# Kernel tuning notes

Measured on AMD Instinct MI355X. Metric: run time of the kernel, lower is better.

## Reference

```python
import jax, jax.numpy as jnp
import numpy as np

NUM_ANCHORS = 400_000
NUM_GTS = 64
NUM_CLASSES = 1
TOPK = 10
ALPHA = 1.0
BETA = 6.0
IMG = 640.0


def setup_inputs() -> dict:
    key = jax.random.key(0)
    k1, k2, k3, k4, k5, k6 = jax.random.split(key, 6)
    # anchor points uniformly over the image plane
    anc_points = jax.random.uniform(k1, (NUM_ANCHORS, 2), jnp.float32, 0.0, IMG)
    # predicted boxes: centered near the anchor point, valid xyxy
    pd_wh = jax.random.uniform(k2, (NUM_ANCHORS, 2), jnp.float32, 8.0, 96.0)
    pd_bboxes = jnp.concatenate([anc_points - pd_wh * 0.5, anc_points + pd_wh * 0.5], axis=-1)
    # predicted class scores in [0, 1] (post-sigmoid)
    pd_scores = jax.random.uniform(k3, (NUM_ANCHORS, NUM_CLASSES), jnp.float32)
    # GT boxes: random centers / sizes, valid xyxy
    gt_c = jax.random.uniform(k4, (NUM_GTS, 2), jnp.float32, 64.0, IMG - 64.0)
    gt_wh = jax.random.uniform(k5, (NUM_GTS, 2), jnp.float32, 16.0, 128.0)
    gt_bboxes = jnp.concatenate([gt_c - gt_wh * 0.5, gt_c + gt_wh * 0.5], axis=-1)
    gt_labels = jax.random.randint(k6, (NUM_GTS,), 0, NUM_CLASSES, dtype=jnp.int32)
    return {
        "pd_scores": pd_scores,
        "pd_bboxes": pd_bboxes,
        "anc_points": anc_points,
        "gt_labels": gt_labels,
        "gt_bboxes": gt_bboxes,
    }


def _box_iou(b1, b2):
    # b1: [A,4] xyxy, b2: [G,4] xyxy -> [A,G] pairwise IoU (torchvision box_iou math)
    lt = jnp.maximum(b1[:, None, :2], b2[None, :, :2])  # [A,G,2]
    rb = jnp.minimum(b1[:, None, 2:], b2[None, :, 2:])  # [A,G,2]
    wh = jnp.clip(rb - lt, 0.0)
    inter = wh[..., 0] * wh[..., 1]                      # [A,G]
    area1 = (b1[:, 2] - b1[:, 0]) * (b1[:, 3] - b1[:, 1])
    area2 = (b2[:, 2] - b2[:, 0]) * (b2[:, 3] - b2[:, 1])
    return inter / (area1[:, None] + area2[None, :] - inter)


def reference(pd_scores, pd_bboxes, anc_points, gt_labels, gt_bboxes):
    A = anc_points.shape[0]
    G = gt_bboxes.shape[0]
    # is anchor point inside each GT box -> [A,G] bool
    x, y = anc_points[:, 0:1], anc_points[:, 1:2]
    is_in_gts = ((x >= gt_bboxes[None, :, 0]) & (x <= gt_bboxes[None, :, 2]) &
                 (y >= gt_bboxes[None, :, 1]) & (y <= gt_bboxes[None, :, 3]))
    # Original gathers candidate anchors (inside >=1 GT) then computes metrics.
    # Equivalent dense form: non-candidates have is_in_gts row all-False so their
    # alignment metric is 0 for every GT and they are filtered by metric>0 below.
    iou = _box_iou(pd_bboxes, gt_bboxes)                         # [A,G]
    cls_scores = pd_scores[:, gt_labels]                          # [A,G]
    cls_scores = cls_scores * is_in_gts.astype(cls_scores.dtype)
    metric = (cls_scores ** ALPHA) * (iou ** BETA)                # [A,G]
    # per-GT top-k anchors by alignment metric
    _, topk_idx = jax.lax.top_k(metric.T, TOPK)                   # [G,k]
    topk_mask = jnp.zeros((A, G), dtype=bool)
    topk_mask = topk_mask.at[topk_idx.T, jnp.arange(G)[None, :]].set(True)
    topk_mask = topk_mask & (metric > 0)
    is_assigned = topk_mask.any(axis=1)                           # [A]
    best_gt = jnp.argmax(metric, axis=1)                          # [A]
    fg_mask = is_assigned
    assigned_gt_idx = jnp.where(fg_mask, best_gt, 0).astype(jnp.int32)
    return fg_mask, assigned_gt_idx
```

## Files before the change

kernel.cpp:

```cpp
#include <hip/hip_runtime.h>

#define NUM_A    400000
#define NUM_G    64
#define TOPK     10
#define CHUNKS   64
#define CHUNK_SZ (NUM_A / CHUNKS)
#define GGROUP   4
#define NGROUPS  (NUM_G / GGROUP)
#define CAP      768

__device__ __forceinline__ bool better(float m1, int a1, float m2, int a2) {
    return (m1 > m2) || ((m1 == m2) && (a1 < a2));
}

__device__ __forceinline__ float iou_metric(
    float px1, float py1, float px2, float py2, float parea, float score,
    float gx1, float gy1, float gx2, float gy2, float garea)
{
    float ltx = fmaxf(px1, gx1);
    float lty = fmaxf(py1, gy1);
    float rbx = fminf(px2, gx2);
    float rby = fminf(py2, gy2);
    float w = fmaxf(rbx - ltx, 0.0f);
    float h = fmaxf(rby - lty, 0.0f);
    float inter = w * h;
    float iou = inter / (parea + garea - inter);
    float iou2 = iou * iou;
    float iou6 = iou2 * iou2 * iou2;
    return score * iou6;
}

__global__ __launch_bounds__(256) void topk_partial_kernel(
    const float* __restrict__ pd_scores,
    const float* __restrict__ pd_bboxes,
    const float* __restrict__ anc_points,
    const float* __restrict__ gt_bboxes,
    float* __restrict__ pval,
    int*   __restrict__ pidx)
{
    const int c   = blockIdx.x;
    const int gg  = blockIdx.y;
    const int tid = threadIdx.x;
    const int g0  = gg * GGROUP;

    __shared__ int   s_cnt[GGROUP];
    __shared__ int   s_cand[GGROUP][CAP];
    __shared__ float s_mv[GGROUP * 64 * TOPK];
    __shared__ int   s_mi[GGROUP * 64 * TOPK];

    if (tid < GGROUP) s_cnt[tid] = 0;

    float gx1[GGROUP], gy1[GGROUP], gx2[GGROUP], gy2[GGROUP];
#pragma unroll
    for (int j = 0; j < GGROUP; ++j) {
        float4 gb = ((const float4*)gt_bboxes)[g0 + j];
        gx1[j] = gb.x; gy1[j] = gb.y; gx2[j] = gb.z; gy2[j] = gb.w;
    }
    __syncthreads();

    const int p0 = c * (CHUNK_SZ / 2);
    const int p1 = p0 + CHUNK_SZ / 2;
    for (int p = p0 + tid; p < p1; p += 256) {
        float4 aq = ((const float4*)anc_points)[p];
        const int a2 = 2 * p;
#pragma unroll
        for (int j = 0; j < GGROUP; ++j) {
            bool in0 = (aq.x >= gx1[j]) && (aq.x <= gx2[j]) &&
                       (aq.y >= gy1[j]) && (aq.y <= gy2[j]);
            bool in1 = (aq.z >= gx1[j]) && (aq.z <= gx2[j]) &&
                       (aq.w >= gy1[j]) && (aq.w <= gy2[j]);
            if (in0) { int q = atomicAdd(&s_cnt[j], 1); if (q < CAP) s_cand[j][q] = a2; }
            if (in1) { int q = atomicAdd(&s_cnt[j], 1); if (q < CAP) s_cand[j][q] = a2 + 1; }
        }
    }
    __syncthreads();

    const int wj   = tid >> 6;
    const int lane = tid & 63;

    float4 gb = ((const float4*)gt_bboxes)[g0 + wj];
    const float garea = (gb.z - gb.x) * (gb.w - gb.y);
    const int n = min(s_cnt[wj], CAP);

    float tv[TOPK]; int ti[TOPK];
#pragma unroll
    for (int k = 0; k < TOPK; ++k) { tv[k] = 0.0f; ti[k] = 0x7fffffff; }

    for (int i = lane; i < n; i += 64) {
        const int a = s_cand[wj][i];
        float4 pb = ((const float4*)pd_bboxes)[a];
        float sc = pd_scores[a];
        float parea = (pb.z - pb.x) * (pb.w - pb.y);
        float m = iou_metric(pb.x, pb.y, pb.z, pb.w, parea, sc,
                             gb.x, gb.y, gb.z, gb.w, garea);
        if (better(m, a, tv[TOPK - 1], ti[TOPK - 1])) {
#pragma unroll
            for (int k = TOPK - 1; k >= 1; --k) {
                bool gp = better(m, a, tv[k - 1], ti[k - 1]);
                bool gc = better(m, a, tv[k],     ti[k]);
                tv[k] = gp ? tv[k - 1] : (gc ? m : tv[k]);
                ti[k] = gp ? ti[k - 1] : (gc ? a : ti[k]);
            }
            if (better(m, a, tv[0], ti[0])) { tv[0] = m; ti[0] = a; }
        }
    }

#pragma unroll
    for (int k = 0; k < TOPK; ++k) {
        s_mv[(wj * 64 + lane) * TOPK + k] = tv[k];
        s_mi[(wj * 64 + lane) * TOPK + k] = ti[k];
    }
    for (int off = 32; off >= 1; off >>= 1) {
        __syncthreads();
        if (lane < off) {
            const int rA = (wj * 64 + lane) * TOPK;
            const int rB = (wj * 64 + lane + off) * TOPK;
            float mv[TOPK]; int mi[TOPK];
            int ia = 0, ib = 0;
#pragma unroll
            for (int k = 0; k < TOPK; ++k) {
                float va = s_mv[rA + ia], vb = s_mv[rB + ib];
                int   na = s_mi[rA + ia], nb = s_mi[rB + ib];
                bool tA = better(va, na, vb, nb);
                mv[k] = tA ? va : vb;
                mi[k] = tA ? na : nb;
                ia += tA ? 1 : 0;
                ib += tA ? 0 : 1;
            }
#pragma unroll
            for (int k = 0; k < TOPK; ++k) { s_mv[rA + k] = mv[k]; s_mi[rA + k] = mi[k]; }
        }
    }
    __syncthreads();
    if (lane < TOPK) {
        const int g = g0 + wj;
        pval[(g * CHUNKS + c) * TOPK + lane] = s_mv[wj * 64 * TOPK + lane];
        pidx[(g * CHUNKS + c) * TOPK + lane] = s_mi[wj * 64 * TOPK + lane];
    }
}

__global__ __launch_bounds__(64) void merge_scatter_kernel(
    const float* __restrict__ pval,
    const int*   __restrict__ pidx,
    int* __restrict__ out_fg,
    int* __restrict__ win_slots)
{
    const int g   = blockIdx.x;
    const int tid = threadIdx.x;

    __shared__ float sv[CHUNKS * TOPK];
    __shared__ int   si[CHUNKS * TOPK];

    const float* pv = pval + (g * CHUNKS + tid) * TOPK;
    const int*   pi = pidx + (g * CHUNKS + tid) * TOPK;
#pragma unroll
    for (int k = 0; k < TOPK; ++k) {
        sv[tid * TOPK + k] = pv[k];
        si[tid * TOPK + k] = pi[k];
    }
    for (int off = CHUNKS / 2; off >= 1; off >>= 1) {
        __syncthreads();
        if (tid < off) {
            const int rA = tid * TOPK, rB = (tid + off) * TOPK;
            float mv[TOPK]; int mi[TOPK];
            int ia = 0, ib = 0;
#pragma unroll
            for (int k = 0; k < TOPK; ++k) {
                float va = sv[rA + ia], vb = sv[rB + ib];
                int   na = si[rA + ia], nb = si[rB + ib];
                bool tA = better(va, na, vb, nb);
                mv[k] = tA ? va : vb;
                mi[k] = tA ? na : nb;
                ia += tA ? 1 : 0;
                ib += tA ? 0 : 1;
            }
#pragma unroll
            for (int k = 0; k < TOPK; ++k) { sv[rA + k] = mv[k]; si[rA + k] = mi[k]; }
        }
    }
    __syncthreads();
    if (tid < TOPK) {
        const bool win = sv[tid] > 0.0f;
        const int  a   = si[tid];
        if (win) out_fg[a] = 1;
        win_slots[g * TOPK + tid] = win ? a : -1;
    }
}

__global__ __launch_bounds__(64) void argmax_flagged_kernel(
    const float* __restrict__ pd_scores,
    const float* __restrict__ pd_bboxes,
    const float* __restrict__ anc_points,
    const float* __restrict__ gt_bboxes,
    const int* __restrict__ win_slots,
    int* __restrict__ out_idx)
{
    __shared__ float4 s_gt[NUM_G];
    __shared__ float  s_ga[NUM_G];
    const int tid = threadIdx.x;
    {
        float4 gb = ((const float4*)gt_bboxes)[tid];
        s_gt[tid] = gb;
        s_ga[tid] = (gb.z - gb.x) * (gb.w - gb.y);
    }
    __syncthreads();

    const int a = win_slots[blockIdx.x * 64 + tid];
    if (a < 0) return;

    float2 ap = ((const float2*)anc_points)[a];
    float4 pb = ((const float4*)pd_bboxes)[a];
    float sc = pd_scores[a];
    float parea = (pb.z - pb.x) * (pb.w - pb.y);

    float best = 0.0f;
    int bidx = 0;
    for (int g = 0; g < NUM_G; ++g) {
        float4 gb = s_gt[g];
        bool in = (ap.x >= gb.x) && (ap.x <= gb.z) &&
                  (ap.y >= gb.y) && (ap.y <= gb.w);
        float m = iou_metric(pb.x, pb.y, pb.z, pb.w, parea,
                             in ? sc : 0.0f,
                             gb.x, gb.y, gb.z, gb.w, s_ga[g]);
        if (m > best) { best = m; bidx = g; }
    }
    out_idx[a] = bidx;
}

extern "C" void kernel_launch(void* const* d_in, const int* in_sizes, int n_in,
                              void* d_out, int out_size, void* d_ws, size_t ws_size,
                              hipStream_t stream) {
    const float* pd_scores  = (const float*)d_in[0];
    const float* pd_bboxes  = (const float*)d_in[1];
    const float* anc_points = (const float*)d_in[2];
    const float* gt_bboxes  = (const float*)d_in[4];

    const int npairs = NUM_G * CHUNKS * TOPK;
    float* pval      = (float*)d_ws;
    int*   pidx      = (int*)(pval + npairs);
    int*   win_slots = (int*)(pidx + npairs);

    int* out_fg  = (int*)d_out;
    int* out_idx = out_fg + NUM_A;

    hipMemsetAsync(d_out, 0, 2 * NUM_A * sizeof(int), stream);

    dim3 g1(CHUNKS, NGROUPS);
    topk_partial_kernel<<<g1, 256, 0, stream>>>(
        pd_scores, pd_bboxes, anc_points, gt_bboxes, pval, pidx);
    merge_scatter_kernel<<<NUM_G, 64, 0, stream>>>(pval, pidx, out_fg, win_slots);
    argmax_flagged_kernel<<<NUM_G * TOPK / 64, 64, 0, stream>>>(
        pd_scores, pd_bboxes, anc_points, gt_bboxes, win_slots, out_idx);
}
```

Measured before the change: 112.1 us.

## Replace shared-memory top-k merge trees with wave shuffle selection and fuse argmax kernel

Within each wave, the per-lane top-10 lists are now merged by ten rounds of shuffle-based max selection instead of a log-depth shared-memory merge tree with block barriers. The merge kernel uses the same shuffle selection. It also computes the best-GT argmax for each winner, with each lane evaluating one GT, so the separate argmax kernel and its launch go away. This cuts shared memory, barriers and one launch, in exchange for more shuffle rounds. Several GTs may pick the same anchor, but they write identical values.

After: 104.5 us, median of 2. 6.8% less time.

```diff
diff --git a/kernel.cpp b/kernel.cpp
--- a/kernel.cpp
+++ b/kernel.cpp
@@ -8,6 +8,7 @@
 #define GGROUP   4
 #define NGROUPS  (NUM_G / GGROUP)
 #define CAP      768
+#define SENT_I   0x7fffffff
 
 __device__ __forceinline__ bool better(float m1, int a1, float m2, int a2) {
     return (m1 > m2) || ((m1 == m2) && (a1 < a2));
@@ -30,6 +31,15 @@
     return score * iou6;
 }
 
+__device__ __forceinline__ void wave_max_pair(float& bv, int& bi) {
+#pragma unroll
+    for (int s = 1; s < 64; s <<= 1) {
+        float ov = __shfl_xor(bv, s, 64);
+        int   oi = __shfl_xor(bi, s, 64);
+        if (better(ov, oi, bv, bi)) { bv = ov; bi = oi; }
+    }
+}
+
 __global__ __launch_bounds__(256) void topk_partial_kernel(
     const float* __restrict__ pd_scores,
     const float* __restrict__ pd_bboxes,
@@ -43,10 +53,8 @@
     const int tid = threadIdx.x;
     const int g0  = gg * GGROUP;
 
-    __shared__ int   s_cnt[GGROUP];
-    __shared__ int   s_cand[GGROUP][CAP];
-    __shared__ float s_mv[GGROUP * 64 * TOPK];
-    __shared__ int   s_mi[GGROUP * 64 * TOPK];
+    __shared__ int s_cnt[GGROUP];
+    __shared__ int s_cand[GGROUP][CAP];
 
     if (tid < GGROUP) s_cnt[tid] = 0;
 
@@ -84,7 +92,7 @@
 
     float tv[TOPK]; int ti[TOPK];
 #pragma unroll
-    for (int k = 0; k < TOPK; ++k) { tv[k] = 0.0f; ti[k] = 0x7fffffff; }
+    for (int k = 0; k < TOPK; ++k) { tv[k] = 0.0f; ti[k] = SENT_I; }
 
     for (int i = lane; i < n; i += 64) {
         const int a = s_cand[wj][i];
@@ -105,126 +113,82 @@
         }
     }
 
+    float outv = 0.0f; int outi = SENT_I;
 #pragma unroll
     for (int k = 0; k < TOPK; ++k) {
-        s_mv[(wj * 64 + lane) * TOPK + k] = tv[k];
-        s_mi[(wj * 64 + lane) * TOPK + k] = ti[k];
-    }
-    for (int off = 32; off >= 1; off >>= 1) {
-        __syncthreads();
-        if (lane < off) {
-            const int rA = (wj * 64 + lane) * TOPK;
-            const int rB = (wj * 64 + lane + off) * TOPK;
-            float mv[TOPK]; int mi[TOPK];
-            int ia = 0, ib = 0;
-#pragma unroll
-            for (int k = 0; k < TOPK; ++k) {
-                float va = s_mv[rA + ia], vb = s_mv[rB + ib];
-                int   na = s_mi[rA + ia], nb = s_mi[rB + ib];
-                bool tA = better(va, na, vb, nb);
-                mv[k] = tA ? va : vb;
-                mi[k] = tA ? na : nb;
-                ia += tA ? 1 : 0;
-                ib += tA ? 0 : 1;
-            }
-#pragma unroll
-            for (int k = 0; k < TOPK; ++k) { s_mv[rA + k] = mv[k]; s_mi[rA + k] = mi[k]; }
-        }
-    }
-    __syncthreads();
+        float bv = tv[0]; int bi = ti[0];
+        wave_max_pair(bv, bi);
+        bool win = (ti[0] == bi);
+#pragma unroll
+        for (int j = 0; j < TOPK - 1; ++j) {
+            tv[j] = win ? tv[j + 1] : tv[j];
+            ti[j] = win ? ti[j + 1] : ti[j];
+        }
+        if (win) { tv[TOPK - 1] = 0.0f; ti[TOPK - 1] = SENT_I; }
+        if (lane == k) { outv = bv; outi = bi; }
+    }
     if (lane < TOPK) {
         const int g = g0 + wj;
-        pval[(g * CHUNKS + c) * TOPK + lane] = s_mv[wj * 64 * TOPK + lane];
-        pidx[(g * CHUNKS + c) * TOPK + lane] = s_mi[wj * 64 * TOPK + lane];
-    }
-}
-
-__global__ __launch_bounds__(64) void merge_scatter_kernel(
+        pval[(g * CHUNKS + c) * TOPK + lane] = outv;
+        pidx[(g * CHUNKS + c) * TOPK + lane] = outi;
+    }
+}
+
+__global__ __launch_bounds__(64) void merge_assign_kernel(
     const float* __restrict__ pval,
     const int*   __restrict__ pidx,
-    int* __restrict__ out_fg,
-    int* __restrict__ win_slots)
-{
-    const int g   = blockIdx.x;
-    const int tid = threadIdx.x;
-
-    __shared__ float sv[CHUNKS * TOPK];
-    __shared__ int   si[CHUNKS * TOPK];
-
-    const float* pv = pval + (g * CHUNKS + tid) * TOPK;
-    const int*   pi = pidx + (g * CHUNKS + tid) * TOPK;
-#pragma unroll
-    for (int k = 0; k < TOPK; ++k) {
-        sv[tid * TOPK + k] = pv[k];
-        si[tid * TOPK + k] = pi[k];
-    }
-    for (int off = CHUNKS / 2; off >= 1; off >>= 1) {
-        __syncthreads();
-        if (tid < off) {
-            const int rA = tid * TOPK, rB = (tid + off) * TOPK;
-            float mv[TOPK]; int mi[TOPK];
-            int ia = 0, ib = 0;
-#pragma unroll
-            for (int k = 0; k < TOPK; ++k) {
-                float va = sv[rA + ia], vb = sv[rB + ib];
-                int   na = si[rA + ia], nb = si[rB + ib];
-                bool tA = better(va, na, vb, nb);
-                mv[k] = tA ? va : vb;
-                mi[k] = tA ? na : nb;
-                ia += tA ? 1 : 0;
-                ib += tA ? 0 : 1;
-            }
-#pragma unroll
-            for (int k = 0; k < TOPK; ++k) { sv[rA + k] = mv[k]; si[rA + k] = mi[k]; }
-        }
-    }
-    __syncthreads();
-    if (tid < TOPK) {
-        const bool win = sv[tid] > 0.0f;
-        const int  a   = si[tid];
-        if (win) out_fg[a] = 1;
-        win_slots[g * TOPK + tid] = win ? a : -1;
-    }
-}
-
-__global__ __launch_bounds__(64) void argmax_flagged_kernel(
     const float* __restrict__ pd_scores,
     const float* __restrict__ pd_bboxes,
     const float* __restrict__ anc_points,
     const float* __restrict__ gt_bboxes,
-    const int* __restrict__ win_slots,
+    int* __restrict__ out_fg,
     int* __restrict__ out_idx)
 {
-    __shared__ float4 s_gt[NUM_G];
-    __shared__ float  s_ga[NUM_G];
-    const int tid = threadIdx.x;
-    {
-        float4 gb = ((const float4*)gt_bboxes)[tid];
-        s_gt[tid] = gb;
-        s_ga[tid] = (gb.z - gb.x) * (gb.w - gb.y);
-    }
-    __syncthreads();
-
-    const int a = win_slots[blockIdx.x * 64 + tid];
-    if (a < 0) return;
-
-    float2 ap = ((const float2*)anc_points)[a];
-    float4 pb = ((const float4*)pd_bboxes)[a];
-    float sc = pd_scores[a];
-    float parea = (pb.z - pb.x) * (pb.w - pb.y);
-
-    float best = 0.0f;
-    int bidx = 0;
-    for (int g = 0; g < NUM_G; ++g) {
-        float4 gb = s_gt[g];
-        bool in = (ap.x >= gb.x) && (ap.x <= gb.z) &&
-                  (ap.y >= gb.y) && (ap.y <= gb.w);
-        float m = iou_metric(pb.x, pb.y, pb.z, pb.w, parea,
-                             in ? sc : 0.0f,
-                             gb.x, gb.y, gb.z, gb.w, s_ga[g]);
-        if (m > best) { best = m; bidx = g; }
-    }
-    out_idx[a] = bidx;
+    const int g    = blockIdx.x;
+    const int lane = threadIdx.x;
+
+    float4 mygt = ((const float4*)gt_bboxes)[lane];
+    float  myga = (mygt.z - mygt.x) * (mygt.w - mygt.y);
+
+    float tv[TOPK]; int ti[TOPK];
+    const float* pv = pval + (g * CHUNKS + lane) * TOPK;
+    const int*   pi = pidx + (g * CHUNKS + lane) * TOPK;
+#pragma unroll
+    for (int k = 0; k < TOPK; ++k) { tv[k] = pv[k]; ti[k] = pi[k]; }
+
+#pragma unroll
+    for (int k = 0; k < TOPK; ++k) {
+        float bv = tv[0]; int bi = ti[0];
+        wave_max_pair(bv, bi);
+        bool win = (ti[0] == bi);
+#pragma unroll
+        for (int j = 0; j < TOPK - 1; ++j) {
+            tv[j] = win ? tv[j + 1] : tv[j];
+            ti[j] = win ? ti[j + 1] : ti[j];
+        }
+        if (win) { tv[TOPK - 1] = 0.0f; ti[TOPK - 1] = SENT_I; }
+
+        if (bv > 0.0f) {
+            const int a = bi;
+            float2 ap = ((const float2*)anc_points)[a];
+            float4 pb = ((const float4*)pd_bboxes)[a];
+            float  sc = pd_scores[a];
+            float parea = (pb.z - pb.x) * (pb.w - pb.y);
+            bool in = (ap.x >= mygt.x) && (ap.x <= mygt.z) &&
+                      (ap.y >= mygt.y) && (ap.y <= mygt.w);
+            float m = iou_metric(pb.x, pb.y, pb.z, pb.w, parea,
+                                 in ? sc : 0.0f,
+                                 mygt.x, mygt.y, mygt.z, mygt.w, myga);
+            float av = m; int ag = lane;
+#pragma unroll
+            for (int s = 1; s < 64; s <<= 1) {
+                float ov = __shfl_xor(av, s, 64);
+                int   og = __shfl_xor(ag, s, 64);
+                if ((ov > av) || ((ov == av) && (og < ag))) { av = ov; ag = og; }
+            }
+            if (lane == 0) { out_fg[a] = 1; out_idx[a] = ag; }
+        }
+    }
 }
 
 extern "C" void kernel_launch(void* const* d_in, const int* in_sizes, int n_in,
@@ -236,9 +200,8 @@
     const float* gt_bboxes  = (const float*)d_in[4];
 
     const int npairs = NUM_G * CHUNKS * TOPK;
-    float* pval      = (float*)d_ws;
-    int*   pidx      = (int*)(pval + npairs);
-    int*   win_slots = (int*)(pidx + npairs);
+    float* pval = (float*)d_ws;
+    int*   pidx = (int*)(pval + npairs);
 
     int* out_fg  = (int*)d_out;
     int* out_idx = out_fg + NUM_A;
@@ -248,7 +211,7 @@
     dim3 g1(CHUNKS, NGROUPS);
     topk_partial_kernel<<<g1, 256, 0, stream>>>(
         pd_scores, pd_bboxes, anc_points, gt_bboxes, pval, pidx);
-    merge_scatter_kernel<<<NUM_G, 64, 0, stream>>>(pval, pidx, out_fg, win_slots);
-    argmax_flagged_kernel<<<NUM_G * TOPK / 64, 64, 0, stream>>>(
-        pd_scores, pd_bboxes, anc_points, gt_bboxes, win_slots, out_idx);
-}
+    merge_assign_kernel<<<NUM_G, 64, 0, stream>>>(
+        pval, pidx, pd_scores, pd_bboxes, anc_points, gt_bboxes,
+        out_fg, out_idx);
+}
```
